# Kernel optimization log

Hardware: AMD Instinct MI355X
Metric: run time of the kernel (lower is better)

The kernel has to match this reference:

```python
import jax, jax.numpy as jnp
import numpy as np

B, N, K = 1, 200000, 16
C_IN = 3          # input feature channels (first layer)
C_MID = 16        # weightnet out_channel
HIDDEN = [8, 8]   # weightnet hidden units
LAST_CH = C_IN + 3  # USE_PE concat of 3-d relative coords
C_OUT = 64


def setup_inputs() -> dict:
    key = jax.random.key(0)
    ks = jax.random.split(key, 16)
    dense_xyz = jax.random.normal(ks[0], (B, N, 3), dtype=jnp.float32)
    dense_feats = jax.random.normal(ks[1], (B, N, C_IN), dtype=jnp.float32)
    nei_inds = jax.random.randint(ks[2], (B, N, K), 0, N)
    # WeightNet: Linear_BN(3->8) -> ReLU -> Linear_BN(8->8) -> ReLU -> Linear_BN(8->16) -> ReLU
    # BN in inference mode is a per-channel affine (gamma, beta).
    def lin(k, i, o):
        return jax.random.normal(k, (i, o), dtype=jnp.float32) * (1.0 / np.sqrt(i))
    wn_w1 = lin(ks[3], 3, HIDDEN[0]);  wn_g1 = jnp.ones((HIDDEN[0],)); wn_b1 = jnp.zeros((HIDDEN[0],))
    wn_w2 = lin(ks[4], HIDDEN[0], HIDDEN[1]); wn_g2 = jnp.ones((HIDDEN[1],)); wn_b2 = jnp.zeros((HIDDEN[1],))
    wn_w3 = lin(ks[5], HIDDEN[1], C_MID); wn_g3 = jnp.ones((C_MID,)); wn_b3 = jnp.zeros((C_MID,))
    lin_w = lin(ks[6], LAST_CH * C_MID, C_OUT)
    lin_b = jnp.zeros((C_OUT,), dtype=jnp.float32)
    return dict(dense_xyz=dense_xyz, dense_feats=dense_feats, nei_inds=nei_inds,
                wn_w1=wn_w1, wn_g1=wn_g1, wn_b1=wn_b1,
                wn_w2=wn_w2, wn_g2=wn_g2, wn_b2=wn_b2,
                wn_w3=wn_w3, wn_g3=wn_g3, wn_b3=wn_b3,
                lin_w=lin_w, lin_b=lin_b)


def _weightnet(x, w1, g1, b1, w2, g2, b2, w3, g3, b3):
    # x: [B, N, K, 3] -> [B, N, K, C_MID]; Linear->BN(affine)->ReLU per layer
    h = jax.nn.relu(jnp.einsum('bnki,io->bnko', x, w1) * g1 + b1)
    h = jax.nn.relu(jnp.einsum('bnki,io->bnko', h, w2) * g2 + b2)
    h = jax.nn.relu(jnp.einsum('bnki,io->bnko', h, w3) * g3 + b3)
    return h


def reference(dense_xyz, dense_feats, nei_inds,
              wn_w1, wn_g1, wn_b1, wn_w2, wn_g2, wn_b2, wn_w3, wn_g3, wn_b3,
              lin_w, lin_b):
    Bq, Nq, _ = dense_xyz.shape
    # gather kNN neighbors: [B, N, K, 3] / [B, N, K, C_IN]
    gathered_xyz = jax.vmap(lambda pts, idx: pts[idx])(dense_xyz, nei_inds)
    localized_xyz = gathered_xyz - dense_xyz[:, :, None, :]   # relative coords
    weightNetInput = localized_xyz                             # USE_VI = False
    gathered_feat = jax.vmap(lambda f, idx: f[idx])(dense_feats, nei_inds)
    # USE_PE: concat relative coords -> [B, N, K, LAST_CH]
    gathered_feat = jnp.concatenate([gathered_feat, weightNetInput], axis=-1)
    weights = _weightnet(weightNetInput, wn_w1, wn_g1, wn_b1,
                         wn_w2, wn_g2, wn_b2, wn_w3, wn_g3, wn_b3)  # [B,N,K,C_MID]
    # feat^T @ weights over K: [B, N, LAST_CH, C_MID] -> flatten c-major
    new_feat = jnp.einsum('bnkc,bnkw->bncw', gathered_feat, weights)
    new_feat = new_feat.reshape(Bq, Nq, -1)
    new_feat = jax.nn.relu(new_feat @ lin_w + lin_b)  # dropout p=0 => identity
    return new_feat, weightNetInput
```

## Files before the change

kernel.cpp:

```cpp
#include <hip/hip_runtime.h>


constexpr int K     = 16;
constexpr int C_OUT = 64;
constexpr int ACC   = 96;

typedef float f32x4 __attribute__((ext_vector_type(4)));

__global__ __launch_bounds__(256, 2) void pointconv_fused(
    const float* __restrict__ xyz,
    const float* __restrict__ feats,
    const int*   __restrict__ nei,
    const float* __restrict__ w1, const float* __restrict__ g1, const float* __restrict__ b1,
    const float* __restrict__ w2, const float* __restrict__ g2, const float* __restrict__ b2,
    const float* __restrict__ w3, const float* __restrict__ g3, const float* __restrict__ b3,
    const float* __restrict__ lw,
    const float* __restrict__ lb,
    float* __restrict__ out_feat,
    float* __restrict__ out_wni,
    int n_pts)
{
    __shared__ float slw[ACC * C_OUT];
    __shared__ float slb[C_OUT];

    const int tid = threadIdx.x;

    {
        const f32x4* src = reinterpret_cast<const f32x4*>(lw);
        f32x4*       dst = reinterpret_cast<f32x4*>(slw);
#pragma unroll
        for (int i = 0; i < (ACC * C_OUT / 4) / 256; ++i)
            dst[tid + i * 256] = src[tid + i * 256];
        if (tid < C_OUT / 4)
            reinterpret_cast<f32x4*>(slb)[tid] =
                reinterpret_cast<const f32x4*>(lb)[tid];
    }
    __syncthreads();

    const int n = blockIdx.x * blockDim.x + tid;
    if (n >= n_pts) return;

    const float cx = xyz[n * 3 + 0];
    const float cy = xyz[n * 3 + 1];
    const float cz = xyz[n * 3 + 2];

    int idx[K];
    {
        const int4* p = reinterpret_cast<const int4*>(nei + (size_t)n * K);
        int4 a = p[0], b = p[1], c = p[2], d = p[3];
        idx[0] = a.x; idx[1] = a.y; idx[2]  = a.z; idx[3]  = a.w;
        idx[4] = b.x; idx[5] = b.y; idx[6]  = b.z; idx[7]  = b.w;
        idx[8] = c.x; idx[9] = c.y; idx[10] = c.z; idx[11] = c.w;
        idx[12] = d.x; idx[13] = d.y; idx[14] = d.z; idx[15] = d.w;
    }

    float acc[ACC];
#pragma unroll
    for (int i = 0; i < ACC; ++i) acc[i] = 0.f;

    float lxyz[K * 3];

#pragma unroll
    for (int k = 0; k < K; ++k) {
        const int j = idx[k];
        const float nx = xyz[(size_t)j * 3 + 0];
        const float ny = xyz[(size_t)j * 3 + 1];
        const float nz = xyz[(size_t)j * 3 + 2];
        const float f0 = feats[(size_t)j * 3 + 0];
        const float f1 = feats[(size_t)j * 3 + 1];
        const float f2 = feats[(size_t)j * 3 + 2];

        const float lx = nx - cx;
        const float ly = ny - cy;
        const float lz = nz - cz;

        lxyz[k * 3 + 0] = lx;
        lxyz[k * 3 + 1] = ly;
        lxyz[k * 3 + 2] = lz;

        float h1[8];
#pragma unroll
        for (int o = 0; o < 8; ++o) {
            float s = lx * w1[o] + ly * w1[8 + o] + lz * w1[16 + o];
            h1[o] = fmaxf(fmaf(s, g1[o], b1[o]), 0.f);
        }
        float h2[8];
#pragma unroll
        for (int o = 0; o < 8; ++o) {
            float s = 0.f;
#pragma unroll
            for (int i = 0; i < 8; ++i) s = fmaf(h1[i], w2[i * 8 + o], s);
            h2[o] = fmaxf(fmaf(s, g2[o], b2[o]), 0.f);
        }
        float h3[16];
#pragma unroll
        for (int o = 0; o < 16; ++o) {
            float s = 0.f;
#pragma unroll
            for (int i = 0; i < 8; ++i) s = fmaf(h2[i], w3[i * 16 + o], s);
            h3[o] = fmaxf(fmaf(s, g3[o], b3[o]), 0.f);
        }

        const float c0 = f0, c1 = f1, c2 = f2, c3 = lx, c4 = ly, c5 = lz;
#pragma unroll
        for (int w = 0; w < 16; ++w) {
            const float h = h3[w];
            acc[0 * 16 + w] = fmaf(c0, h, acc[0 * 16 + w]);
            acc[1 * 16 + w] = fmaf(c1, h, acc[1 * 16 + w]);
            acc[2 * 16 + w] = fmaf(c2, h, acc[2 * 16 + w]);
            acc[3 * 16 + w] = fmaf(c3, h, acc[3 * 16 + w]);
            acc[4 * 16 + w] = fmaf(c4, h, acc[4 * 16 + w]);
            acc[5 * 16 + w] = fmaf(c5, h, acc[5 * 16 + w]);
        }
    }

    {
        f32x4* wp = reinterpret_cast<f32x4*>(out_wni + (size_t)n * (K * 3));
#pragma unroll
        for (int t = 0; t < 12; ++t) {
            f32x4 v = { lxyz[4 * t + 0], lxyz[4 * t + 1],
                        lxyz[4 * t + 2], lxyz[4 * t + 3] };
            wp[t] = v;
        }
    }

#pragma unroll 1
    for (int ch = 0; ch < 4; ++ch) {
        const int o0 = ch * 16;
        float o16[16];
#pragma unroll
        for (int t = 0; t < 16; ++t) o16[t] = slb[o0 + t];
#pragma unroll
        for (int j2 = 0; j2 < ACC; ++j2) {
            const float a = acc[j2];
#pragma unroll
            for (int t = 0; t < 16; ++t)
                o16[t] = fmaf(a, slw[j2 * C_OUT + o0 + t], o16[t]);
        }
        f32x4* op = reinterpret_cast<f32x4*>(out_feat + (size_t)n * 64 + o0);
#pragma unroll
        for (int t = 0; t < 4; ++t) {
            f32x4 v = { fmaxf(o16[4 * t + 0], 0.f),
                        fmaxf(o16[4 * t + 1], 0.f),
                        fmaxf(o16[4 * t + 2], 0.f),
                        fmaxf(o16[4 * t + 3], 0.f) };
            op[t] = v;
        }
    }
}

extern "C" void kernel_launch(void* const* d_in, const int* in_sizes, int n_in,
                              void* d_out, int out_size, void* d_ws, size_t ws_size,
                              hipStream_t stream) {
    const float* xyz   = (const float*)d_in[0];
    const float* feats = (const float*)d_in[1];
    const int*   nei   = (const int*)d_in[2];
    const float* w1 = (const float*)d_in[3];
    const float* g1 = (const float*)d_in[4];
    const float* b1 = (const float*)d_in[5];
    const float* w2 = (const float*)d_in[6];
    const float* g2 = (const float*)d_in[7];
    const float* b2 = (const float*)d_in[8];
    const float* w3 = (const float*)d_in[9];
    const float* g3 = (const float*)d_in[10];
    const float* b3 = (const float*)d_in[11];
    const float* lw = (const float*)d_in[12];
    const float* lb = (const float*)d_in[13];

    const int n_pts = in_sizes[0] / 3;

    float* out = (float*)d_out;
    float* out_feat = out;
    float* out_wni  = out + (size_t)n_pts * C_OUT;

    const int threads = 256;
    const int blocks  = (n_pts + threads - 1) / threads;
    pointconv_fused<<<blocks, threads, 0, stream>>>(
        xyz, feats, nei,
        w1, g1, b1, w2, g2, b2, w3, g3, b3,
        lw, lb, out_feat, out_wni, n_pts);
}
```

Baseline: 352.4 us.

## Stage weightnet params in LDS, stream relative coords, raise occupancy

Copies the weightnet weights, gammas and betas into transposed LDS tables read as vector loads, replacing repeated scalar global loads. Writes the relative-coordinate output every four neighbours instead of holding all 48 values until the end, which cuts register pressure. Raises the launch-bounds occupancy hint from 2 to 3 blocks per SIMD. The risk is spills, since the 96 accumulators must now fit in a tighter register budget, and the interleaved stores may add memory traffic inside the loop.

```diff
diff --git a/kernel.cpp b/kernel.cpp
--- a/kernel.cpp
+++ b/kernel.cpp
@@ -6,8 +6,9 @@
 constexpr int ACC   = 96;
 
 typedef float f32x4 __attribute__((ext_vector_type(4)));
-
-__global__ __launch_bounds__(256, 2) void pointconv_fused(
+typedef float f32x2 __attribute__((ext_vector_type(2)));
+
+__global__ __launch_bounds__(256, 3) void pointconv_fused(
     const float* __restrict__ xyz,
     const float* __restrict__ feats,
     const int*   __restrict__ nei,
@@ -22,6 +23,9 @@
 {
     __shared__ float slw[ACC * C_OUT];
     __shared__ float slb[C_OUT];
+    __shared__ float sL1[8 * 8];
+    __shared__ float sL2[8 * 16];
+    __shared__ float sL3[16 * 12];
 
     const int tid = threadIdx.x;
 
@@ -29,11 +33,28 @@
         const f32x4* src = reinterpret_cast<const f32x4*>(lw);
         f32x4*       dst = reinterpret_cast<f32x4*>(slw);
 #pragma unroll
-        for (int i = 0; i < (ACC * C_OUT / 4) / 256; ++i)
+        for (int i = 0; i < 6; ++i)
             dst[tid + i * 256] = src[tid + i * 256];
         if (tid < C_OUT / 4)
             reinterpret_cast<f32x4*>(slb)[tid] =
                 reinterpret_cast<const f32x4*>(lb)[tid];
+    }
+    if (tid < 8) {
+        sL1[tid * 8 + 0] = w1[0 * 8 + tid];
+        sL1[tid * 8 + 1] = w1[1 * 8 + tid];
+        sL1[tid * 8 + 2] = w1[2 * 8 + tid];
+        sL1[tid * 8 + 3] = g1[tid];
+        sL1[tid * 8 + 4] = b1[tid];
+#pragma unroll
+        for (int i = 0; i < 8; ++i) sL2[tid * 16 + i] = w2[i * 8 + tid];
+        sL2[tid * 16 + 8] = g2[tid];
+        sL2[tid * 16 + 9] = b2[tid];
+    }
+    if (tid < 16) {
+#pragma unroll
+        for (int i = 0; i < 8; ++i) sL3[tid * 12 + i] = w3[i * 16 + tid];
+        sL3[tid * 12 + 8] = g3[tid];
+        sL3[tid * 12 + 9] = b3[tid];
     }
     __syncthreads();
 
@@ -58,7 +79,7 @@
 #pragma unroll
     for (int i = 0; i < ACC; ++i) acc[i] = 0.f;
 
-    float lxyz[K * 3];
+    float lxyz[12];
 
 #pragma unroll
     for (int k = 0; k < K; ++k) {
@@ -74,31 +95,43 @@
         const float ly = ny - cy;
         const float lz = nz - cz;
 
-        lxyz[k * 3 + 0] = lx;
-        lxyz[k * 3 + 1] = ly;
-        lxyz[k * 3 + 2] = lz;
+        lxyz[(k & 3) * 3 + 0] = lx;
+        lxyz[(k & 3) * 3 + 1] = ly;
+        lxyz[(k & 3) * 3 + 2] = lz;
 
         float h1[8];
 #pragma unroll
         for (int o = 0; o < 8; ++o) {
-            float s = lx * w1[o] + ly * w1[8 + o] + lz * w1[16 + o];
-            h1[o] = fmaxf(fmaf(s, g1[o], b1[o]), 0.f);
+            f32x4 r = *reinterpret_cast<const f32x4*>(&sL1[o * 8]);
+            float bb = sL1[o * 8 + 4];
+            float s = lx * r.x + ly * r.y + lz * r.z;
+            h1[o] = fmaxf(fmaf(s, r.w, bb), 0.f);
         }
         float h2[8];
 #pragma unroll
         for (int o = 0; o < 8; ++o) {
-            float s = 0.f;
-#pragma unroll
-            for (int i = 0; i < 8; ++i) s = fmaf(h1[i], w2[i * 8 + o], s);
-            h2[o] = fmaxf(fmaf(s, g2[o], b2[o]), 0.f);
+            f32x4 wa = *reinterpret_cast<const f32x4*>(&sL2[o * 16]);
+            f32x4 wb = *reinterpret_cast<const f32x4*>(&sL2[o * 16 + 4]);
+            f32x2 gb = *reinterpret_cast<const f32x2*>(&sL2[o * 16 + 8]);
+            float s = h1[0] * wa.x;
+            s = fmaf(h1[1], wa.y, s); s = fmaf(h1[2], wa.z, s);
+            s = fmaf(h1[3], wa.w, s); s = fmaf(h1[4], wb.x, s);
+            s = fmaf(h1[5], wb.y, s); s = fmaf(h1[6], wb.z, s);
+            s = fmaf(h1[7], wb.w, s);
+            h2[o] = fmaxf(fmaf(s, gb.x, gb.y), 0.f);
         }
         float h3[16];
 #pragma unroll
         for (int o = 0; o < 16; ++o) {
-            float s = 0.f;
-#pragma unroll
-            for (int i = 0; i < 8; ++i) s = fmaf(h2[i], w3[i * 16 + o], s);
-            h3[o] = fmaxf(fmaf(s, g3[o], b3[o]), 0.f);
+            f32x4 wa = *reinterpret_cast<const f32x4*>(&sL3[o * 12]);
+            f32x4 wb = *reinterpret_cast<const f32x4*>(&sL3[o * 12 + 4]);
+            f32x2 gb = *reinterpret_cast<const f32x2*>(&sL3[o * 12 + 8]);
+            float s = h2[0] * wa.x;
+            s = fmaf(h2[1], wa.y, s); s = fmaf(h2[2], wa.z, s);
+            s = fmaf(h2[3], wa.w, s); s = fmaf(h2[4], wb.x, s);
+            s = fmaf(h2[5], wb.y, s); s = fmaf(h2[6], wb.z, s);
+            s = fmaf(h2[7], wb.w, s);
+            h3[o] = fmaxf(fmaf(s, gb.x, gb.y), 0.f);
         }
 
         const float c0 = f0, c1 = f1, c2 = f2, c3 = lx, c4 = ly, c5 = lz;
@@ -112,15 +145,14 @@
             acc[4 * 16 + w] = fmaf(c4, h, acc[4 * 16 + w]);
             acc[5 * 16 + w] = fmaf(c5, h, acc[5 * 16 + w]);
         }
-    }
-
-    {
-        f32x4* wp = reinterpret_cast<f32x4*>(out_wni + (size_t)n * (K * 3));
-#pragma unroll
-        for (int t = 0; t < 12; ++t) {
-            f32x4 v = { lxyz[4 * t + 0], lxyz[4 * t + 1],
-                        lxyz[4 * t + 2], lxyz[4 * t + 3] };
-            wp[t] = v;
+
+        if ((k & 3) == 3) {
+            f32x4* wp = reinterpret_cast<f32x4*>(
+                out_wni + (size_t)n * (K * 3) + (k - 3) * 3);
+            f32x4 v0 = { lxyz[0], lxyz[1], lxyz[2],  lxyz[3] };
+            f32x4 v1 = { lxyz[4], lxyz[5], lxyz[6],  lxyz[7] };
+            f32x4 v2 = { lxyz[8], lxyz[9], lxyz[10], lxyz[11] };
+            wp[0] = v0; wp[1] = v1; wp[2] = v2;
         }
     }
 
```

New measurement: 553.5 us. 1.57x slower.
